# Kernel tuning notes

Measured on AMD Instinct MI355X. Metric: run time of the kernel, lower is better.

The kernel has to match this reference:

```python
import jax, jax.numpy as jnp
import numpy as np

NUM_HEADS = 4
GROUPS = 8
EPS = 1e-5

def setup_inputs() -> dict:
    key = jax.random.key(0)
    ks = jax.random.split(key, 4)
    C = 256
    x = jax.random.normal(ks[0], (4, C, 64, 64), dtype=jnp.float32)
    qkv_w = jax.random.normal(ks[1], (3 * C, C), dtype=jnp.float32) * (C ** -0.5)
    qkv_b = jnp.zeros((3 * C,), dtype=jnp.float32)
    proj_w = jax.random.normal(ks[2], (C, C), dtype=jnp.float32) * (C ** -0.5)
    proj_b = jnp.zeros((C,), dtype=jnp.float32)
    gamma = jnp.ones((C,), dtype=jnp.float32)
    beta = jnp.zeros((C,), dtype=jnp.float32)
    return {"x": x, "qkv_w": qkv_w, "qkv_b": qkv_b, "proj_w": proj_w, "proj_b": proj_b, "gamma": gamma, "beta": beta}

def group_norm(x, gamma, beta):
    B, C, H, W = x.shape
    xg = x.reshape(B, GROUPS, C // GROUPS, H, W)
    mean = xg.mean(axis=(2, 3, 4), keepdims=True)
    var = xg.var(axis=(2, 3, 4), keepdims=True)
    xn = (xg - mean) * jax.lax.rsqrt(var + EPS)
    xn = xn.reshape(B, C, H, W)
    return xn * gamma[None, :, None, None] + beta[None, :, None, None]

def reference(x, qkv_w, qkv_b, proj_w, proj_b, gamma, beta):
    B, C, H, W = x.shape
    L = H * W
    hd = C // NUM_HEADS
    xn = group_norm(x, gamma, beta)  # (B,C,H,W)
    xf = xn.reshape(B, C, L)  # tokens along last axis
    # 1x1 conv == per-pixel linear: (3C, C) @ (B, C, L)
    qkv = jnp.einsum('oc,bcl->bol', qkv_w, xf) + qkv_b[None, :, None]
    q, k, v = jnp.split(qkv, 3, axis=1)  # each (B,C,L)
    q = q.reshape(B, NUM_HEADS, hd, L)
    k = k.reshape(B, NUM_HEADS, hd, L)
    v = v.reshape(B, NUM_HEADS, hd, L)
    scale = hd ** -0.5
    attn = jnp.einsum('bhdq,bhdk->bhqk', q, k) * scale
    attn = jax.nn.softmax(attn, axis=-1)
    out = jnp.einsum('bhqk,bhdk->bhdq', attn, v)  # (B,h,hd,L)
    out = out.reshape(B, C, L)
    out = jnp.einsum('oc,bcl->bol', proj_w, out) + proj_b[None, :, None]
    return out.reshape(B, C, H, W) + xn
```

## Files before the change

### kernel.cpp

```cpp
#include <hip/hip_runtime.h>
#include <math.h>

#define L 4096
#define LOG2E_O8 0.18033688011112042f

typedef float f32x16 __attribute__((ext_vector_type(16)));
typedef __bf16 bf16x8 __attribute__((ext_vector_type(8)));

static __device__ __forceinline__ float fast_exp2(float x) {
    return __builtin_amdgcn_exp2f(x);
}
static __device__ __forceinline__ unsigned short f2bfu(float f) {
    unsigned int u = __builtin_bit_cast(unsigned int, f);
    u += 0x7fffu + ((u >> 16) & 1u);
    return (unsigned short)(u >> 16);
}
static __device__ __forceinline__ unsigned int cvtpk(float a, float b) {
    unsigned int r;
    asm("v_cvt_pk_bf16_f32 %0, %1, %2" : "=v"(r) : "v"(a), "v"(b));
    return r;
}
static __device__ __forceinline__ void pl32swap(unsigned int& a, unsigned int& b) {
    auto r = __builtin_amdgcn_permlane32_swap(a, b, false, false);
    a = r[0];
    b = r[1];
}
static __device__ __forceinline__ bf16x8 ld_frag_g(const unsigned short* p) {
    uint4 v = *(const uint4*)p;
    return __builtin_bit_cast(bf16x8, v);
}
static __device__ __forceinline__ bf16x8 ld_frag_s(const unsigned short* p) {
    uint4 v = *(const uint4*)p;
    return __builtin_bit_cast(bf16x8, v);
}

__global__ __launch_bounds__(256) void gn_stats_part_kernel(const float* __restrict__ x,
                                                            float2* __restrict__ part) {
    const int blk = blockIdx.x;
    const float4* p = (const float4*)(x + (size_t)blk * 8192);
    float sum = 0.f, sq = 0.f;
    for (int i = threadIdx.x; i < 2048; i += 256) {
        float4 v = p[i];
        sum += (v.x + v.y) + (v.z + v.w);
        sq  += (v.x * v.x + v.y * v.y) + (v.z * v.z + v.w * v.w);
    }
#pragma unroll
    for (int off = 1; off < 64; off <<= 1) {
        sum += __shfl_xor(sum, off);
        sq  += __shfl_xor(sq, off);
    }
    __shared__ float red[8];
    const int t = threadIdx.x;
    if ((t & 63) == 0) { red[(t >> 6) * 2] = sum; red[(t >> 6) * 2 + 1] = sq; }
    __syncthreads();
    if (t == 0) {
        float s = red[0] + red[2] + red[4] + red[6];
        float q = red[1] + red[3] + red[5] + red[7];
        part[blk] = make_float2(s, q);
    }
}

__global__ __launch_bounds__(64) void gn_stats_final_kernel(const float2* __restrict__ part,
                                                            float2* __restrict__ stats) {
    const int bg = threadIdx.x;
    if (bg < 32) {
        float s = 0.f, q = 0.f;
#pragma unroll
        for (int i = 0; i < 16; ++i) {
            float2 v = part[bg * 16 + i];
            s += v.x; q += v.y;
        }
        const float inv_n = 1.0f / (32.0f * L);
        float mean = s * inv_n;
        float var = q * inv_n - mean * mean;
        stats[bg] = make_float2(mean, rsqrtf(var + 1e-5f));
    }
}

__global__ __launch_bounds__(256) void wcvt_kernel(const float* __restrict__ qkv_w,
                                                   const float* __restrict__ proj_w,
                                                   unsigned short* __restrict__ Wqb,
                                                   unsigned short* __restrict__ Wpb) {
    const int i4 = (blockIdx.x * 256 + threadIdx.x) * 4;
    const float* src;
    unsigned short* dst;
    if (i4 < 196608) { src = qkv_w + i4; dst = Wqb + i4; }
    else             { src = proj_w + (i4 - 196608); dst = Wpb + (i4 - 196608); }
    float4 v = *(const float4*)src;
    ushort4 o;
    o.x = f2bfu(v.x); o.y = f2bfu(v.y); o.z = f2bfu(v.z); o.w = f2bfu(v.w);
    *(ushort4*)dst = o;
}

__global__ __launch_bounds__(256) void gn_apply_kernel(const float* __restrict__ x,
                                                       const float* __restrict__ gamma,
                                                       const float* __restrict__ beta,
                                                       const float2* __restrict__ stats,
                                                       unsigned short* __restrict__ xnT) {
    __shared__ float tile[64][68];
    const int t = threadIdx.x;
    const int b = blockIdx.z, c0 = blockIdx.y * 64, l0 = blockIdx.x * 64;
    const int lc = (t & 15) * 4, cr = t >> 4;
#pragma unroll
    for (int p = 0; p < 4; ++p) {
        const int c = c0 + cr + p * 16;
        const float2 st = stats[b * 8 + (c >> 5)];
        const float g = gamma[c] * st.y;
        const float be = beta[c] - st.x * g;
        float4 v = *(const float4*)&x[((size_t)b * 256 + c) * L + l0 + lc];
        float4 o;
        o.x = v.x * g + be; o.y = v.y * g + be; o.z = v.z * g + be; o.w = v.w * g + be;
        *(float4*)&tile[cr + p * 16][lc] = o;
    }
    __syncthreads();
    const int lr = t >> 2, cc = (t & 3) * 16;
    unsigned short* dst = &xnT[((size_t)b * L + l0 + lr) * 256 + c0 + cc];
#pragma unroll
    for (int g4 = 0; g4 < 4; ++g4) {
        ushort4 o4;
        o4.x = f2bfu(tile[cc + g4 * 4 + 0][lr]);
        o4.y = f2bfu(tile[cc + g4 * 4 + 1][lr]);
        o4.z = f2bfu(tile[cc + g4 * 4 + 2][lr]);
        o4.w = f2bfu(tile[cc + g4 * 4 + 3][lr]);
        *(ushort4*)&dst[g4 * 4] = o4;
    }
}

__global__ __launch_bounds__(256) void qkv_gemm_kernel(
        const unsigned short* __restrict__ xnT,
        const unsigned short* __restrict__ Wq,
        const float* __restrict__ bias,
        unsigned short* __restrict__ Qb,
        unsigned short* __restrict__ Kb,
        unsigned short* __restrict__ Vb) {
    const int t = threadIdx.x, lane = t & 63, w = t >> 6;
    const int l5 = lane >> 5, l31 = lane & 31;
    const int wn = w & 1, wm = w >> 1;
    const int n0 = blockIdx.x * 128 + wn * 64;
    const int m0 = blockIdx.y * 128 + wm * 64;
    const int b = blockIdx.z;
    const unsigned short* ap = xnT + ((size_t)b * L + n0 + l31) * 256 + l5 * 8;
    const unsigned short* bp = Wq + (size_t)(m0 + l31) * 256 + l5 * 8;
    f32x16 acc[2][2];
#pragma unroll
    for (int i = 0; i < 2; ++i)
#pragma unroll
        for (int j = 0; j < 2; ++j)
#pragma unroll
            for (int r = 0; r < 16; ++r) acc[i][j][r] = 0.f;
#pragma unroll
    for (int k0 = 0; k0 < 256; k0 += 16) {
        bf16x8 a0 = ld_frag_g(ap + k0);
        bf16x8 a1 = ld_frag_g(ap + 32 * 256 + k0);
        bf16x8 b0 = ld_frag_g(bp + k0);
        bf16x8 b1 = ld_frag_g(bp + 32 * 256 + k0);
        acc[0][0] = __builtin_amdgcn_mfma_f32_32x32x16_bf16(a0, b0, acc[0][0], 0, 0, 0);
        acc[0][1] = __builtin_amdgcn_mfma_f32_32x32x16_bf16(a0, b1, acc[0][1], 0, 0, 0);
        acc[1][0] = __builtin_amdgcn_mfma_f32_32x32x16_bf16(a1, b0, acc[1][0], 0, 0, 0);
        acc[1][1] = __builtin_amdgcn_mfma_f32_32x32x16_bf16(a1, b1, acc[1][1], 0, 0, 0);
    }
    const int sec = m0 >> 8;
    const size_t bh = (size_t)(b * 4 + ((m0 >> 6) & 3));
#pragma unroll
    for (int j = 0; j < 2; ++j) {
        const int m = m0 + j * 32 + l31;
        const int d = m & 63;
        const float bi = bias[m];
        if (sec < 2) {
            unsigned short* dst = (sec ? Kb : Qb) + bh * L * 64 + d;
            const float sc = (sec == 0) ? LOG2E_O8 : 1.0f;
#pragma unroll
            for (int i = 0; i < 2; ++i)
#pragma unroll
                for (int r = 0; r < 16; ++r) {
                    const int n = n0 + i * 32 + (r & 3) + 8 * (r >> 2) + 4 * l5;
                    dst[(size_t)n * 64] = f2bfu((acc[i][j][r] + bi) * sc);
                }
        } else {
            unsigned short* dst = Vb + (bh * 64 + d) * L;
#pragma unroll
            for (int i = 0; i < 2; ++i)
#pragma unroll
                for (int g = 0; g < 4; ++g) {
                    const int n = n0 + i * 32 + 8 * g + 4 * l5;
                    ushort4 st;
                    st.x = f2bfu(acc[i][j][4 * g + 0] + bi);
                    st.y = f2bfu(acc[i][j][4 * g + 1] + bi);
                    st.z = f2bfu(acc[i][j][4 * g + 2] + bi);
                    st.w = f2bfu(acc[i][j][4 * g + 3] + bi);
                    *(ushort4*)&dst[n] = st;
                }
        }
    }
}

__global__ __launch_bounds__(512, 2) void attn_kernel(
        const unsigned short* __restrict__ Qb,
        const unsigned short* __restrict__ Kb,
        const unsigned short* __restrict__ Vb,
        float* __restrict__ Po,
        float* __restrict__ Pl) {
    const int t = threadIdx.x;
    const int lane = t & 63, w = t >> 6;
    const int wq = w & 3, wk = w >> 2;
    const int l5 = lane >> 5, l31 = lane & 31;
    const int n = blockIdx.x;
    const int bh_i = n & 15;
    const int r = n >> 4;
    const int qt = r & 31;
    const int kh = r >> 5;
    const int q0 = qt * 128 + wq * 32;
    const size_t bh = (size_t)bh_i;

    __shared__ alignas(16) char smem[38912];
    auto Kt = (unsigned short(*)[2][32][72])smem;
    auto Vt = (unsigned short(*)[2][64][40])(smem + 18432);
    auto comb = (float(*)[64][36])smem;

    const unsigned short* qp = Qb + (bh * L + q0 + l31) * 64 + l5 * 8;
    bf16x8 qf[4];
#pragma unroll
    for (int dc = 0; dc < 4; ++dc) qf[dc] = ld_frag_g(qp + dc * 16);

    const int ts = t & 255;
    const int kr = ts >> 3, kq = ts & 7;
    const int vd = ts >> 2, vp = ts & 3;
    const int kbase = kh * 2048 + wk * 1024;
    const unsigned short* kgsrc = Kb + bh * L * 64 + (size_t)kbase * 64 + kr * 64 + kq * 8;
    const unsigned short* vgsrc = Vb + (bh * 64 + vd) * L + kbase + vp * 8;

    f32x16 o0, o1;
#pragma unroll
    for (int r2 = 0; r2 < 16; ++r2) { o0[r2] = 0.f; o1[r2] = 0.f; }
    float4 ls = make_float4(0.f, 0.f, 0.f, 0.f);

    {
        uint4 kv = *(const uint4*)kgsrc;
        uint4 vv = *(const uint4*)vgsrc;
        *(uint4*)&Kt[wk][0][kr][kq * 8] = kv;
        *(uint4*)&Vt[wk][0][vd][vp * 8] = vv;
    }
    __syncthreads();

    for (int kc = 0; kc < 32; ++kc) {
        const int buf = kc & 1;
        uint4 knx, vnx;
        if (kc < 31) {
            knx = *(const uint4*)(kgsrc + (size_t)(kc + 1) * 2048);
            vnx = *(const uint4*)(vgsrc + (kc + 1) * 32);
        }
        bf16x8 kf[4], vf[2][2];
#pragma unroll
        for (int dc = 0; dc < 4; ++dc)
            kf[dc] = ld_frag_s(&Kt[wk][buf][l31][dc * 16 + l5 * 8]);
#pragma unroll
        for (int dh = 0; dh < 2; ++dh)
#pragma unroll
            for (int h16 = 0; h16 < 2; ++h16)
                vf[dh][h16] = ld_frag_s(&Vt[wk][buf][dh * 32 + l31][h16 * 16 + l5 * 8]);
        f32x16 s;
#pragma unroll
        for (int r2 = 0; r2 < 16; ++r2) s[r2] = 0.f;
#pragma unroll
        for (int dc = 0; dc < 4; ++dc)
            s = __builtin_amdgcn_mfma_f32_32x32x16_bf16(kf[dc], qf[dc], s, 0, 0, 0);
#pragma unroll
        for (int r2 = 0; r2 < 16; ++r2) s[r2] = fast_exp2(s[r2]);
#pragma unroll
        for (int g = 0; g < 4; ++g) {
            ls.x += s[4 * g + 0];
            ls.y += s[4 * g + 1];
            ls.z += s[4 * g + 2];
            ls.w += s[4 * g + 3];
        }
        unsigned int w0 = cvtpk(s[0],  s[1]);
        unsigned int w1 = cvtpk(s[2],  s[3]);
        unsigned int w2 = cvtpk(s[4],  s[5]);
        unsigned int w3 = cvtpk(s[6],  s[7]);
        unsigned int w4 = cvtpk(s[8],  s[9]);
        unsigned int w5 = cvtpk(s[10], s[11]);
        unsigned int w6 = cvtpk(s[12], s[13]);
        unsigned int w7 = cvtpk(s[14], s[15]);
        pl32swap(w0, w2);
        pl32swap(w1, w3);
        pl32swap(w4, w6);
        pl32swap(w5, w7);
        int4 p0v, p1v;
        p0v.x = (int)w0; p0v.y = (int)w1; p0v.z = (int)w2; p0v.w = (int)w3;
        p1v.x = (int)w4; p1v.y = (int)w5; p1v.z = (int)w6; p1v.w = (int)w7;
        bf16x8 pb0 = __builtin_bit_cast(bf16x8, p0v);
        bf16x8 pb1 = __builtin_bit_cast(bf16x8, p1v);
        o0 = __builtin_amdgcn_mfma_f32_32x32x16_bf16(vf[0][0], pb0, o0, 0, 0, 0);
        o0 = __builtin_amdgcn_mfma_f32_32x32x16_bf16(vf[0][1], pb1, o0, 0, 0, 0);
        o1 = __builtin_amdgcn_mfma_f32_32x32x16_bf16(vf[1][0], pb0, o1, 0, 0, 0);
        o1 = __builtin_amdgcn_mfma_f32_32x32x16_bf16(vf[1][1], pb1, o1, 0, 0, 0);
        if (kc < 31) {
            *(uint4*)&Kt[wk][buf ^ 1][kr][kq * 8] = knx;
            *(uint4*)&Vt[wk][buf ^ 1][vd][vp * 8] = vnx;
        }
        __syncthreads();
    }
    float lrun = (ls.x + ls.y) + (ls.z + ls.w);
    lrun += __shfl_xor(lrun, 32);

    if (wk == 1) {
        float* cb = comb[wq][lane];
#pragma unroll
        for (int g = 0; g < 4; ++g) {
            *(float4*)&cb[4 * g] =
                make_float4(o0[4 * g + 0], o0[4 * g + 1], o0[4 * g + 2], o0[4 * g + 3]);
            *(float4*)&cb[16 + 4 * g] =
                make_float4(o1[4 * g + 0], o1[4 * g + 1], o1[4 * g + 2], o1[4 * g + 3]);
        }
        cb[32] = lrun;
    }
    __syncthreads();
    if (wk == 0) {
        const float* cb = comb[wq][lane];
#pragma unroll
        for (int r2 = 0; r2 < 16; ++r2) { o0[r2] += cb[r2]; o1[r2] += cb[16 + r2]; }
        lrun += cb[32];
        float* pp = Po + ((size_t)(kh * 16 + bh_i) * 4096 + q0 + l31) * 64 + 4 * l5;
#pragma unroll
        for (int g = 0; g < 4; ++g) {
            *(float4*)&pp[8 * g] =
                make_float4(o0[4 * g + 0], o0[4 * g + 1], o0[4 * g + 2], o0[4 * g + 3]);
            *(float4*)&pp[32 + 8 * g] =
                make_float4(o1[4 * g + 0], o1[4 * g + 1], o1[4 * g + 2], o1[4 * g + 3]);
        }
        if (l5 == 0) Pl[(size_t)(kh * 16 + bh_i) * 4096 + q0 + l31] = lrun;
    }
}

__global__ __launch_bounds__(256) void attn_merge_kernel(
        const float* __restrict__ Po,
        const float* __restrict__ Pl,
        unsigned short* __restrict__ aoT) {
    const int t = threadIdx.x;
    const int ri = blockIdx.x * 64 + (t >> 2);
    const int d0 = (t & 3) * 16;
    const int bh = ri >> 12, q = ri & 4095;
    const int b = bh >> 2, h = bh & 3;
    const float l0 = Pl[ri], l1 = Pl[65536 + ri];
    const float inv = 1.f / (l0 + l1);
    const float* p0 = Po + (size_t)ri * 64 + d0;
    const float* p1 = p0 + (size_t)65536 * 64;
    unsigned short* op = aoT + ((size_t)b * L + q) * 256 + h * 64 + d0;
#pragma unroll
    for (int g = 0; g < 2; ++g) {
        float4 a0 = *(const float4*)&p0[g * 8 + 0];
        float4 a1 = *(const float4*)&p0[g * 8 + 4];
        float4 c0 = *(const float4*)&p1[g * 8 + 0];
        float4 c1 = *(const float4*)&p1[g * 8 + 4];
        uint4 st;
        st.x = cvtpk((a0.x + c0.x) * inv, (a0.y + c0.y) * inv);
        st.y = cvtpk((a0.z + c0.z) * inv, (a0.w + c0.w) * inv);
        st.z = cvtpk((a1.x + c1.x) * inv, (a1.y + c1.y) * inv);
        st.w = cvtpk((a1.z + c1.z) * inv, (a1.w + c1.w) * inv);
        *(uint4*)&op[g * 8] = st;
    }
}

__global__ __launch_bounds__(256) void proj_gemm_kernel(
        const unsigned short* __restrict__ aoT,
        const unsigned short* __restrict__ Wp,
        const float* __restrict__ bias,
        const float* __restrict__ x,
        const float* __restrict__ gamma,
        const float* __restrict__ beta,
        const float2* __restrict__ stats,
        float* __restrict__ out) {
    const int t = threadIdx.x, lane = t & 63, w = t >> 6;
    const int l5 = lane >> 5, l31 = lane & 31;
    const int wn = w & 1, wm = w >> 1;
    const int n0 = blockIdx.x * 64 + wn * 32;
    const int m0 = blockIdx.y * 128 + wm * 64;
    const int b = blockIdx.z;
    const unsigned short* ap = aoT + ((size_t)b * L + n0 + l31) * 256 + l5 * 8;
    const unsigned short* bp = Wp + (size_t)(m0 + l31) * 256 + l5 * 8;
    f32x16 acc[2];
#pragma unroll
    for (int j = 0; j < 2; ++j)
#pragma unroll
        for (int r = 0; r < 16; ++r) acc[j][r] = 0.f;
#pragma unroll
    for (int k0 = 0; k0 < 256; k0 += 16) {
        bf16x8 a  = ld_frag_g(ap + k0);
        bf16x8 b0 = ld_frag_g(bp + k0);
        bf16x8 b1 = ld_frag_g(bp + 32 * 256 + k0);
        acc[0] = __builtin_amdgcn_mfma_f32_32x32x16_bf16(a, b0, acc[0], 0, 0, 0);
        acc[1] = __builtin_amdgcn_mfma_f32_32x32x16_bf16(a, b1, acc[1], 0, 0, 0);
    }
#pragma unroll
    for (int j = 0; j < 2; ++j) {
        const int co = m0 + j * 32 + l31;
        const float2 st = stats[b * 8 + (co >> 5)];
        const float g = gamma[co] * st.y;
        const float be = beta[co] - st.x * g + bias[co];
        const float* xr = &x[((size_t)b * 256 + co) * L];
        float* orow = &out[((size_t)b * 256 + co) * L];
#pragma unroll
        for (int q = 0; q < 4; ++q) {
            const int n = n0 + 8 * q + 4 * l5;
            float4 xv = *(const float4*)&xr[n];
            float4 ov;
            ov.x = acc[j][4 * q + 0] + (xv.x * g + be);
            ov.y = acc[j][4 * q + 1] + (xv.y * g + be);
            ov.z = acc[j][4 * q + 2] + (xv.z * g + be);
            ov.w = acc[j][4 * q + 3] + (xv.w * g + be);
            *(float4*)&orow[n] = ov;
        }
    }
}

extern "C" void kernel_launch(void* const* d_in, const int* in_sizes, int n_in,
                              void* d_out, int out_size, void* d_ws, size_t ws_size,
                              hipStream_t stream) {
    const float* x      = (const float*)d_in[0];
    const float* qkv_w  = (const float*)d_in[1];
    const float* qkv_b  = (const float*)d_in[2];
    const float* proj_w = (const float*)d_in[3];
    const float* proj_b = (const float*)d_in[4];
    const float* gamma  = (const float*)d_in[5];
    const float* beta   = (const float*)d_in[6];
    float* out = (float*)d_out;

    char* ws = (char*)d_ws;
    float2* stats       = (float2*)ws;
    unsigned short* Wqb = (unsigned short*)(ws + 512);
    unsigned short* Wpb = (unsigned short*)(ws + 512 + 393216);
    unsigned short* xnT = (unsigned short*)(ws + 524800);
    unsigned short* Qb  = (unsigned short*)(ws + 524800 + 8388608);
    unsigned short* Kb  = Qb + (size_t)16 * L * 64;
    unsigned short* Vb  = Kb + (size_t)16 * L * 64;
    unsigned short* aoT = Vb + (size_t)16 * L * 64;
    float* Po           = (float*)(ws + 42467840);
    float* Pl           = (float*)(ws + 42467840 + 33554432);
    float2* spart       = (float2*)(ws + 524800);

    gn_stats_part_kernel<<<dim3(512), dim3(256), 0, stream>>>(x, spart);
    gn_stats_final_kernel<<<dim3(1), dim3(64), 0, stream>>>(spart, stats);
    wcvt_kernel<<<dim3(256), dim3(256), 0, stream>>>(qkv_w, proj_w, Wqb, Wpb);
    gn_apply_kernel<<<dim3(64, 4, 4), dim3(256), 0, stream>>>(x, gamma, beta, stats, xnT);
    qkv_gemm_kernel<<<dim3(32, 6, 4), dim3(256), 0, stream>>>(xnT, Wqb, qkv_b, Qb, Kb, Vb);
    attn_kernel<<<dim3(1024), dim3(512), 0, stream>>>(Qb, Kb, Vb, Po, Pl);
    attn_merge_kernel<<<dim3(1024), dim3(256), 0, stream>>>(Po, Pl, aoT);
    proj_gemm_kernel<<<dim3(64, 2, 4), dim3(256), 0, stream>>>(aoT, Wpb, proj_b, x, gamma, beta, stats, out);
}
```

Baseline: 226.1 us.

## Fuse key-split attention merge into attention kernel with 1024-thread blocks

The attention kernel now covers all four key quarters inside one 1024-thread block, reducing partial outputs through shared memory in two stages and writing normalized bf16 output directly. This removes the separate merge kernel and the fp32 partial-output round trip through global memory (Po/Pl). In exchange the grid halves to 512 blocks, shared memory doubles, and there is an extra block-wide barrier, which can lower occupancy and parallelism.

```diff
diff --git a/kernel.cpp b/kernel.cpp
--- a/kernel.cpp
+++ b/kernel.cpp
@@ -194,28 +194,26 @@
     }
 }
 
-__global__ __launch_bounds__(512, 2) void attn_kernel(
+__global__ __launch_bounds__(1024, 4) void attn_kernel(
         const unsigned short* __restrict__ Qb,
         const unsigned short* __restrict__ Kb,
         const unsigned short* __restrict__ Vb,
-        float* __restrict__ Po,
-        float* __restrict__ Pl) {
+        unsigned short* __restrict__ aoT) {
     const int t = threadIdx.x;
     const int lane = t & 63, w = t >> 6;
     const int wq = w & 3, wk = w >> 2;
     const int l5 = lane >> 5, l31 = lane & 31;
     const int n = blockIdx.x;
     const int bh_i = n & 15;
-    const int r = n >> 4;
-    const int qt = r & 31;
-    const int kh = r >> 5;
+    const int qt = n >> 4;
+    const int b = bh_i >> 2, h = bh_i & 3;
     const int q0 = qt * 128 + wq * 32;
     const size_t bh = (size_t)bh_i;
 
-    __shared__ alignas(16) char smem[38912];
+    __shared__ alignas(16) char smem[77824];
     auto Kt = (unsigned short(*)[2][32][72])smem;
-    auto Vt = (unsigned short(*)[2][64][40])(smem + 18432);
-    auto comb = (float(*)[64][36])smem;
+    auto Vt = (unsigned short(*)[2][64][40])(smem + 36864);
+    auto comb = (float(*)[4][64][36])smem;
 
     const unsigned short* qp = Qb + (bh * L + q0 + l31) * 64 + l5 * 8;
     bf16x8 qf[4];
@@ -225,7 +223,7 @@
     const int ts = t & 255;
     const int kr = ts >> 3, kq = ts & 7;
     const int vd = ts >> 2, vp = ts & 3;
-    const int kbase = kh * 2048 + wk * 1024;
+    const int kbase = wk * 1024;
     const unsigned short* kgsrc = Kb + bh * L * 64 + (size_t)kbase * 64 + kr * 64 + kq * 8;
     const unsigned short* vgsrc = Vb + (bh * 64 + vd) * L + kbase + vp * 8;
 
@@ -303,8 +301,8 @@
     float lrun = (ls.x + ls.y) + (ls.z + ls.w);
     lrun += __shfl_xor(lrun, 32);
 
-    if (wk == 1) {
-        float* cb = comb[wq][lane];
+    if (wk & 1) {
+        float* cb = comb[wk >> 1][wq][lane];
 #pragma unroll
         for (int g = 0; g < 4; ++g) {
             *(float4*)&cb[4 * g] =
@@ -315,49 +313,42 @@
         cb[32] = lrun;
     }
     __syncthreads();
-    if (wk == 0) {
-        const float* cb = comb[wq][lane];
+    if (!(wk & 1)) {
+        const float* cb = comb[wk >> 1][wq][lane];
 #pragma unroll
         for (int r2 = 0; r2 < 16; ++r2) { o0[r2] += cb[r2]; o1[r2] += cb[16 + r2]; }
         lrun += cb[32];
-        float* pp = Po + ((size_t)(kh * 16 + bh_i) * 4096 + q0 + l31) * 64 + 4 * l5;
+        if (wk == 2) {
+            float* cw = comb[1][wq][lane];
+#pragma unroll
+            for (int g = 0; g < 4; ++g) {
+                *(float4*)&cw[4 * g] =
+                    make_float4(o0[4 * g + 0], o0[4 * g + 1], o0[4 * g + 2], o0[4 * g + 3]);
+                *(float4*)&cw[16 + 4 * g] =
+                    make_float4(o1[4 * g + 0], o1[4 * g + 1], o1[4 * g + 2], o1[4 * g + 3]);
+            }
+            cw[32] = lrun;
+        }
+    }
+    __syncthreads();
+    if (wk == 0) {
+        const float* cb = comb[1][wq][lane];
+#pragma unroll
+        for (int r2 = 0; r2 < 16; ++r2) { o0[r2] += cb[r2]; o1[r2] += cb[16 + r2]; }
+        lrun += cb[32];
+        const float inv = 1.f / lrun;
+        unsigned short* op = aoT + ((size_t)b * L + q0 + l31) * 256 + h * 64 + 4 * l5;
 #pragma unroll
         for (int g = 0; g < 4; ++g) {
-            *(float4*)&pp[8 * g] =
-                make_float4(o0[4 * g + 0], o0[4 * g + 1], o0[4 * g + 2], o0[4 * g + 3]);
-            *(float4*)&pp[32 + 8 * g] =
-                make_float4(o1[4 * g + 0], o1[4 * g + 1], o1[4 * g + 2], o1[4 * g + 3]);
-        }
-        if (l5 == 0) Pl[(size_t)(kh * 16 + bh_i) * 4096 + q0 + l31] = lrun;
-    }
-}
-
-__global__ __launch_bounds__(256) void attn_merge_kernel(
-        const float* __restrict__ Po,
-        const float* __restrict__ Pl,
-        unsigned short* __restrict__ aoT) {
-    const int t = threadIdx.x;
-    const int ri = blockIdx.x * 64 + (t >> 2);
-    const int d0 = (t & 3) * 16;
-    const int bh = ri >> 12, q = ri & 4095;
-    const int b = bh >> 2, h = bh & 3;
-    const float l0 = Pl[ri], l1 = Pl[65536 + ri];
-    const float inv = 1.f / (l0 + l1);
-    const float* p0 = Po + (size_t)ri * 64 + d0;
-    const float* p1 = p0 + (size_t)65536 * 64;
-    unsigned short* op = aoT + ((size_t)b * L + q) * 256 + h * 64 + d0;
-#pragma unroll
-    for (int g = 0; g < 2; ++g) {
-        float4 a0 = *(const float4*)&p0[g * 8 + 0];
-        float4 a1 = *(const float4*)&p0[g * 8 + 4];
-        float4 c0 = *(const float4*)&p1[g * 8 + 0];
-        float4 c1 = *(const float4*)&p1[g * 8 + 4];
-        uint4 st;
-        st.x = cvtpk((a0.x + c0.x) * inv, (a0.y + c0.y) * inv);
-        st.y = cvtpk((a0.z + c0.z) * inv, (a0.w + c0.w) * inv);
-        st.z = cvtpk((a1.x + c1.x) * inv, (a1.y + c1.y) * inv);
-        st.w = cvtpk((a1.z + c1.z) * inv, (a1.w + c1.w) * inv);
-        *(uint4*)&op[g * 8] = st;
+            uint2 st;
+            st.x = cvtpk(o0[4 * g + 0] * inv, o0[4 * g + 1] * inv);
+            st.y = cvtpk(o0[4 * g + 2] * inv, o0[4 * g + 3] * inv);
+            *(uint2*)&op[8 * g] = st;
+            uint2 st2;
+            st2.x = cvtpk(o1[4 * g + 0] * inv, o1[4 * g + 1] * inv);
+            st2.y = cvtpk(o1[4 * g + 2] * inv, o1[4 * g + 3] * inv);
+            *(uint2*)&op[32 + 8 * g] = st2;
+        }
     }
 }
 
@@ -434,8 +425,6 @@
     unsigned short* Kb  = Qb + (size_t)16 * L * 64;
     unsigned short* Vb  = Kb + (size_t)16 * L * 64;
     unsigned short* aoT = Vb + (size_t)16 * L * 64;
-    float* Po           = (float*)(ws + 42467840);
-    float* Pl           = (float*)(ws + 42467840 + 33554432);
     float2* spart       = (float2*)(ws + 524800);
 
     gn_stats_part_kernel<<<dim3(512), dim3(256), 0, stream>>>(x, spart);
@@ -443,7 +432,6 @@
     wcvt_kernel<<<dim3(256), dim3(256), 0, stream>>>(qkv_w, proj_w, Wqb, Wpb);
     gn_apply_kernel<<<dim3(64, 4, 4), dim3(256), 0, stream>>>(x, gamma, beta, stats, xnT);
     qkv_gemm_kernel<<<dim3(32, 6, 4), dim3(256), 0, stream>>>(xnT, Wqb, qkv_b, Qb, Kb, Vb);
-    attn_kernel<<<dim3(1024), dim3(512), 0, stream>>>(Qb, Kb, Vb, Po, Pl);
-    attn_merge_kernel<<<dim3(1024), dim3(256), 0, stream>>>(Po, Pl, aoT);
+    attn_kernel<<<dim3(512), dim3(1024), 0, stream>>>(Qb, Kb, Vb, aoT);
     proj_gemm_kernel<<<dim3(64, 2, 4), dim3(256), 0, stream>>>(aoT, Wpb, proj_b, x, gamma, beta, stats, out);
 }
```

Measured after the change: 224.2 us. No clear change (-0.8%).
